# Kernel tuning notes

Hardware: AMD Instinct MI355X
Metric: run time of the kernel (lower is better)

## Reference

```python
import jax, jax.numpy as jnp
import numpy as np

N_HEADS = 8
B, TS, SEG, D, FACTOR, DFF = 4, 64, 128, 256, 10, 1024


def sparsemax(z):
    # projection onto the simplex along the last axis (Martins & Astudillo 2016)
    d = z.shape[-1]
    z_sorted = -jnp.sort(-z, axis=-1)                      # descending
    k = jnp.arange(1, d + 1, dtype=z.dtype)
    z_cum = jnp.cumsum(z_sorted, axis=-1)
    support = (1.0 + k * z_sorted) > z_cum
    k_z = jnp.sum(support.astype(jnp.int32), axis=-1, keepdims=True)
    tau = (jnp.take_along_axis(z_cum, k_z - 1, axis=-1) - 1.0) / k_z.astype(z.dtype)
    return jnp.maximum(z - tau, 0.0)


def _hopf(q_in, k_in, wq, bq, wk, bk, wv, bv, wo, bo):
    # Faithful Hopfield block. NOTE: original torch code ignores the `values`
    # argument -- values are value_projection(key_projection(keys)).
    b, L, _ = q_in.shape
    S = k_in.shape[1]
    q = (q_in @ wq + bq).reshape(b, L, N_HEADS, -1)
    kproj = k_in @ wk + bk
    v = (kproj @ wv + bv).reshape(b, S, N_HEADS, -1)
    kk = kproj.reshape(b, S, N_HEADS, -1)
    scale = 1.0 / np.sqrt(q.shape[-1]).astype(np.float32)
    A = sparsemax(jnp.einsum('blhe,bshe->bhls', q, kk) * scale)
    out = jnp.einsum('bhls,bshd->blhd', A, v)
    # mix=True: transpose(2,1).contiguous().view(B, L, -1) quirk
    out = jnp.swapaxes(out, 1, 2).reshape(b, L, -1)
    return out @ wo + bo


def _mlp(h, w1, b1, w2, b2):
    return jax.nn.gelu(h @ w1 + b1, approximate=False) @ w2 + b2


def _ln(h, g, b, eps=1e-5):
    m = jnp.mean(h, axis=-1, keepdims=True)
    v = jnp.var(h, axis=-1, keepdims=True)
    return (h - m) / jnp.sqrt(v + eps) * g + b


def setup_inputs() -> dict:
    key = jax.random.key(0)
    ks = jax.random.split(key, 24)
    i = 0
    inp = {}
    inp['x'] = jax.random.normal(ks[i], (B, TS, SEG, D), jnp.float32); i += 1
    for pfx in ('ct', 'cs', 'hp'):
        for nm in ('q', 'k', 'v', 'o'):
            inp[f'{pfx}_w{nm}'] = jax.random.normal(ks[i], (D, D), jnp.float32) * 0.02; i += 1
            inp[f'{pfx}_b{nm}'] = jnp.zeros((D,), jnp.float32)
    inp['cs_key'] = jax.random.normal(ks[i], (1, FACTOR, D), jnp.float32) * 0.02; i += 1
    inp['ln_g'] = jnp.ones((D,), jnp.float32)
    inp['ln_b'] = jnp.zeros((D,), jnp.float32)
    for mp in ('mlp1', 'mlp2'):
        inp[f'{mp}_w1'] = jax.random.normal(ks[i], (D, DFF), jnp.float32) * 0.02; i += 1
        inp[f'{mp}_b1'] = jnp.zeros((DFF,), jnp.float32)
        inp[f'{mp}_w2'] = jax.random.normal(ks[i], (DFF, D), jnp.float32) * 0.02; i += 1
        inp[f'{mp}_b2'] = jnp.zeros((D,), jnp.float32)
    return inp


def reference(x, ct_wq, ct_bq, ct_wk, ct_bk, ct_wv, ct_bv, ct_wo, ct_bo,
              cs_wq, cs_bq, cs_wk, cs_bk, cs_wv, cs_bv, cs_wo, cs_bo, cs_key,
              hp_wq, hp_bq, hp_wk, hp_bk, hp_wv, hp_bv, hp_wo, hp_bo,
              ln_g, ln_b, mlp1_w1, mlp1_b1, mlp1_w2, mlp1_b2,
              mlp2_w1, mlp2_b1, mlp2_w2, mlp2_b2):
    b, ts, seg, d = x.shape
    time_in = x.reshape(b * ts, seg, d)
    time_enc = _hopf(time_in, time_in, ct_wq, ct_bq, ct_wk, ct_bk, ct_wv, ct_bv, ct_wo, ct_bo)
    dim_in = time_in + time_enc
    dim_in = dim_in + _mlp(dim_in, mlp1_w1, mlp1_b1, mlp1_w2, mlp1_b2)
    # (b ts) seg d -> (b seg) ts d
    series_in = dim_in.reshape(b, ts, seg, d).transpose(0, 2, 1, 3).reshape(b * seg, ts, d)
    kmat = jnp.broadcast_to(cs_key, (b * seg, cs_key.shape[1], d))
    series_h = _hopf(series_in, kmat, cs_wq, cs_bq, cs_wk, cs_bk, cs_wv, cs_bv, cs_wo, cs_bo)
    # original passes series_h as `values` but Hopfield.forward ignores it
    pooled_h = _hopf(series_in, series_in, hp_wq, hp_bq, hp_wk, hp_bk, hp_wv, hp_bv, hp_wo, hp_bo)
    dim_enc = _ln(series_h + pooled_h, ln_g, ln_b)
    dim_enc = dim_enc + _mlp(dim_enc, mlp2_w1, mlp2_b1, mlp2_w2, mlp2_b2)
    return dim_enc.reshape(b, seg, ts, d).transpose(0, 2, 1, 3)
```

## Files before the change

### kernel.cpp

```cpp
#include <hip/hip_runtime.h>
#include <math.h>


typedef unsigned short u16;
typedef unsigned int u32;
typedef __attribute__((ext_vector_type(8))) short s8v;
typedef __attribute__((ext_vector_type(4))) float f4v;

#define MFMA16 __builtin_amdgcn_mfma_f32_16x16x32_bf16

#define ASYNC16(lds, g) __builtin_amdgcn_global_load_lds( \
    (const __attribute__((address_space(1))) unsigned int*)(const void*)(g), \
    (__attribute__((address_space(3))) unsigned int*)(void*)(lds), 16, 0, 0)

__device__ __forceinline__ float gelu_exact(float x) {
    return 0.5f * x * (1.0f + erff(x * 0.70710678118654752f));
}
__device__ __forceinline__ u16 bf16_rne(float f) {
    u32 u = __float_as_uint(f);
    return (u16)((u + 0x7FFFu + ((u >> 16) & 1u)) >> 16);
}
__device__ __forceinline__ float bf16_to_f(u16 h) {
    return __uint_as_float((u32)h << 16);
}

struct WB {
    const float* src[14];
    u16* dst[14];
    int K[14], N[14];
};
__global__ __launch_bounds__(256)
void wconv_batch(WB wb)
{
    __shared__ float tile[32][33];
    const int mi = blockIdx.y;
    const int K = wb.K[mi], N = wb.N[mi];
    const int tilesN = N >> 5;
    if ((int)blockIdx.x >= tilesN * (K >> 5)) return;
    const int n0 = (blockIdx.x % tilesN) * 32, k0 = (blockIdx.x / tilesN) * 32;
    const float* W = wb.src[mi];
    u16* Wh = wb.dst[mi];
    const int t = threadIdx.x;
    const int r = t >> 3, c = (t & 7) << 2;
    const float4 f = *(const float4*)&W[(size_t)(k0 + r) * N + n0 + c];
    tile[r][c] = f.x; tile[r][c + 1] = f.y; tile[r][c + 2] = f.z; tile[r][c + 3] = f.w;
    __syncthreads();
    u32 hp[2];
    #pragma unroll
    for (int p = 0; p < 2; ++p) {
        const u16 h0 = bf16_rne(tile[c + p * 2][r]);
        const u16 h1 = bf16_rne(tile[c + p * 2 + 1][r]);
        hp[p] = (u32)h0 | ((u32)h1 << 16);
    }
    uint2 hv; hv.x = hp[0]; hv.y = hp[1];
    *(uint2*)&Wh[(size_t)(n0 + r) * K + k0 + c] = hv;
}

__global__ __launch_bounds__(256)
void conv_hi(const float* __restrict__ x, u16* __restrict__ xh)
{
    const size_t base = ((size_t)blockIdx.x * 256 + threadIdx.x) * 8;
    const float4 a = *(const float4*)(x + base);
    const float4 b = *(const float4*)(x + base + 4);
    const float fs[8] = {a.x, a.y, a.z, a.w, b.x, b.y, b.z, b.w};
    __align__(16) u16 hh[8];
    #pragma unroll
    for (int i = 0; i < 8; ++i) hh[i] = bf16_rne(fs[i]);
    *(uint4*)(xh + base) = *(const uint4*)hh;
}

__global__ __launch_bounds__(256)
void bias_concat(const float* a0, const float* a1, float* o1,
                 const float* b0, const float* b1, const float* b2, float* o2)
{
    const int t = threadIdx.x;
    o1[t] = a0[t]; o1[256 + t] = a1[t];
    o2[t] = b0[t]; o2[256 + t] = b1[t]; o2[512 + t] = b2[t];
}

template<int GELU, int RES, int OUTMODE>
__global__ __launch_bounds__(256)
void gemm_bf16(const u16* __restrict__ A, int lda, const u16* __restrict__ W,
               const float* __restrict__ bias, const float* __restrict__ Rf,
               u16* __restrict__ Cb, float* __restrict__ Cf,
               int M, int N, int K)
{
    __shared__ __align__(16) u16 SM[128 * 136];
    u16* const As = SM;
    u16* const Ws = SM + 128 * 64;
    const int t = threadIdx.x;
    const int bm = blockIdx.x, bn = blockIdx.y;
    const int w = t >> 6, lane = t & 63;
    const int wy = w >> 1, wx = w & 1;
    const int lm = lane & 15, quad = lane >> 4, kq = quad << 3;
    const int srow = lane >> 3;
    const int scol = (((lane & 7) ^ srow) << 3);
    const u16* gA = A + (size_t)(bm * 128 + w * 32 + srow) * lda + scol;
    const u16* gW = W + (size_t)(bn * 128 + w * 32 + srow) * K + scol;
    f4v acc[4][4] = {};
    for (int k0 = 0; k0 < K; k0 += 64) {
        #pragma unroll
        for (int r8 = 0; r8 < 4; ++r8) {
            ASYNC16(&As[(w * 32 + r8 * 8) * 64], gA + k0 + (size_t)(r8 * 8) * lda);
            ASYNC16(&Ws[(w * 32 + r8 * 8) * 64], gW + k0 + (size_t)(r8 * 8) * K);
        }
        __syncthreads();
        #pragma unroll
        for (int ks = 0; ks < 2; ++ks) {
            const int ch = ks * 4 + quad;
            const int sw = ((ch ^ (lm & 7)) << 3);
            s8v fw[4], fa[4];
            #pragma unroll
            for (int i = 0; i < 4; ++i) {
                fw[i] = *(const s8v*)&Ws[(wx * 64 + i * 16 + lm) * 64 + sw];
                fa[i] = *(const s8v*)&As[(wy * 64 + i * 16 + lm) * 64 + sw];
            }
            #pragma unroll
            for (int ic = 0; ic < 4; ++ic)
                #pragma unroll
                for (int jr = 0; jr < 4; ++jr)
                    acc[ic][jr] = MFMA16(fw[ic], fa[jr], acc[ic][jr], 0, 0, 0);
        }
        __syncthreads();
    }
    #pragma unroll
    for (int ic = 0; ic < 4; ++ic) {
        const int cloc = wx * 64 + ic * 16 + (quad << 2);
        const int col0 = bn * 128 + cloc;
        const float4 bv = *(const float4*)&bias[col0];
        #pragma unroll
        for (int jr = 0; jr < 4; ++jr) {
            const int rloc = wy * 64 + jr * 16 + lm;
            const int row = bm * 128 + rloc;
            const size_t o = (size_t)row * N + col0;
            float v[4] = {acc[ic][jr][0] + bv.x, acc[ic][jr][1] + bv.y,
                          acc[ic][jr][2] + bv.z, acc[ic][jr][3] + bv.w};
            if (RES) {
                const float4 rv = *(const float4*)(Rf + o);
                v[0] += rv.x; v[1] += rv.y; v[2] += rv.z; v[3] += rv.w;
            }
            if (GELU) {
                #pragma unroll
                for (int r = 0; r < 4; ++r) v[r] = gelu_exact(v[r]);
            }
            if (OUTMODE != 2) {
                uint2 hp;
                hp.x = (u32)bf16_rne(v[0]) | ((u32)bf16_rne(v[1]) << 16);
                hp.y = (u32)bf16_rne(v[2]) | ((u32)bf16_rne(v[3]) << 16);
                *(uint2*)&SM[rloc * 136 + cloc] = hp;
            }
            if (OUTMODE >= 1) {
                float4 fv; fv.x = v[0]; fv.y = v[1]; fv.z = v[2]; fv.w = v[3];
                *(float4*)(Cf + o) = fv;
            }
        }
    }
    if (OUTMODE != 2) {
        __syncthreads();
        #pragma unroll
        for (int p = 0; p < 8; ++p) {
            const int idx = p * 256 + t;
            const int row = idx >> 4, ch = (idx & 15) << 3;
            *(uint4*)&Cb[(size_t)(bm * 128 + row) * N + bn * 128 + ch] =
                *(const uint4*)&SM[row * 136 + ch];
        }
    }
}

__global__ __launch_bounds__(256)
void gemm_tiny(const float* __restrict__ A, const float* __restrict__ W,
               const float* __restrict__ bias, float* __restrict__ Cf,
               u16* __restrict__ Ch, int K, int N)
{
    __shared__ float red[8][33];
    const int m = blockIdx.x;
    const int ncol = blockIdx.y * 32 + (threadIdx.x & 31);
    const int ks = threadIdx.x >> 5;
    const int kc = K >> 3;
    float p = 0.f;
    for (int k = ks * kc; k < (ks + 1) * kc; ++k)
        p = fmaf(A[(size_t)m * K + k], W[(size_t)k * N + ncol], p);
    red[ks][threadIdx.x & 31] = p;
    __syncthreads();
    if (ks == 0) {
        float s = bias[ncol];
        #pragma unroll
        for (int i = 0; i < 8; ++i) s += red[i][threadIdx.x & 31];
        Cf[(size_t)m * N + ncol] = s;
        if (Ch) Ch[(size_t)m * N + ncol] = bf16_rne(s);
    }
}

__global__ __launch_bounds__(256)
void cs_vt(const float* __restrict__ v2f, u16* __restrict__ VT2)
{
    const int c = threadIdx.x;
    for (int j = 0; j < 32; ++j)
        VT2[c * 32 + j] = (j < 10) ? bf16_rne(v2f[(size_t)j * 256 + c]) : (u16)0;
}

template<int S>
__global__ __launch_bounds__(256)
void transpose_vt(const u16* __restrict__ V, u16* __restrict__ VT)
{
    __shared__ __align__(16) u16 Vs[S * 40];
    const int t = threadIdx.x;
    const int nb = blockIdx.x >> 3, h = blockIdx.x & 7;
    for (int idx = t; idx < S * 4; idx += 256) {
        const int row = idx >> 2, ch = idx & 3;
        *(uint4*)&Vs[row * 40 + ch * 8] =
            *(const uint4*)&V[((size_t)nb * S + row) * 256 + h * 32 + ch * 8];
    }
    __syncthreads();
    for (int idx = t; idx < 32 * S / 8; idx += 256) {
        const int e = idx / (S / 8), seg = idx % (S / 8);
        const int j0 = seg * 8;
        __align__(16) u16 tmp[8];
        #pragma unroll
        for (int i = 0; i < 8; ++i) tmp[i] = Vs[(j0 + i) * 40 + e];
        *(uint4*)&VT[(((size_t)nb * 8 + h) * 32 + e) * S + j0] = *(const uint4*)tmp;
    }
}

template<int L, int S, int SHARED>
__global__ __launch_bounds__(256)
void attn_bf16(const u16* __restrict__ q, int ldq, int qcol0,
               const u16* __restrict__ k, int ldk, int kcol0,
               const u16* __restrict__ VT, u16* __restrict__ ho)
{
    constexpr int S16 = (S + 15) & ~15;
    constexpr int S32 = (S + 31) & ~31;
    constexpr int NT = S16 / 16;
    constexpr int KC = S32 / 32;
    constexpr int LC = L / 64;
    constexpr int SP = S32 + 8;
    __shared__ __align__(16) u16 Qs[64 * 32];
    __shared__ __align__(16) u16 Ks[S16 * 32];
    __shared__ __align__(16) u16 Vs[32 * SP];
    __shared__ __align__(16) u16 Ps[64 * SP];
    const int t = threadIdx.x;
    const int lc = (LC == 1) ? 0 : (blockIdx.x & (LC - 1));
    const int bh = (LC == 1) ? blockIdx.x : (blockIdx.x >> 1);
    const int b = bh >> 3, h = bh & 7;
    const int qrow0 = lc * 64;
    const int w = t >> 6, lane = t & 63;
    const int lm = lane & 15, quad = lane >> 4, kq = quad << 3;

    {
        const int srow = lane >> 2, scol = (lane & 3) << 3;
        const u16* g = q + (size_t)(b * L + qrow0 + w * 16 + srow) * ldq
                         + qcol0 + h * 32 + scol;
        ASYNC16(&Qs[(w * 16) * 32], g);
    }
    if (SHARED) {
        for (int idx = t; idx < S16 * 4; idx += 256) {
            const int row = idx >> 2, ch = idx & 3;
            uint4 val = make_uint4(0, 0, 0, 0);
            if (row < S) val = *(const uint4*)&k[(size_t)row * ldk + kcol0 + h * 32 + ch * 8];
            *(uint4*)&Ks[row * 32 + ch * 8] = val;
        }
    } else {
        const int srow = lane >> 2, scol = (lane & 3) << 3;
        for (int c = w; c < S / 16; c += 4) {
            const u16* g = k + (size_t)(b * S + c * 16 + srow) * ldk
                             + kcol0 + h * 32 + scol;
            ASYNC16(&Ks[(c * 16) * 32], g);
        }
    }
    for (int idx = t; idx < 32 * S32 / 8; idx += 256) {
        const int e = idx / (S32 / 8), ch = idx % (S32 / 8);
        const size_t src = SHARED ? ((size_t)(h * 32 + e) * S32 + ch * 8)
                                  : ((((size_t)b * 8 + h) * 32 + e) * S32 + ch * 8);
        *(uint4*)&Vs[e * SP + ch * 8] = *(const uint4*)&VT[src];
    }
    __syncthreads();

    const s8v fq = *(const s8v*)&Qs[(w * 16 + lm) * 32 + kq];
    f4v zac[NT];
    #pragma unroll
    for (int nt = 0; nt < NT; ++nt) {
        const s8v fk = *(const s8v*)&Ks[(nt * 16 + lm) * 32 + kq];
        zac[nt] = MFMA16(fk, fq, f4v{0.f, 0.f, 0.f, 0.f}, 0, 0, 0);
    }
    const float scale = 0.17677669529663687f;
    float z[NT][4];
    #pragma unroll
    for (int nt = 0; nt < NT; ++nt)
        #pragma unroll
        for (int r = 0; r < 4; ++r) {
            float zz = zac[nt][r] * scale;
            if ((S & 15) && nt * 16 + quad * 4 + r >= S) zz = -3.0e38f;
            z[nt][r] = zz;
        }

    float tau = -3.0e38f, kprev = -1.f;
    for (int it = 0; it <= S; ++it) {
        float sum = 0.f;
        int cnt = 0;
        #pragma unroll
        for (int nt = 0; nt < NT; ++nt)
            #pragma unroll
            for (int r = 0; r < 4; ++r) {
                const bool a = z[nt][r] > tau;
                cnt += a;
                sum += a ? z[nt][r] : 0.f;
            }
        sum += __shfl_xor(sum, 16); cnt += __shfl_xor(cnt, 16);
        sum += __shfl_xor(sum, 32); cnt += __shfl_xor(cnt, 32);
        const float fc = (float)cnt;
        const bool anych = (fc != kprev);
        kprev = fc;
        tau = (sum - 1.f) / fc;
        if (__ballot(anych) == 0ULL) break;
    }

    u16* const Prow = &Ps[(w * 16 + lm) * SP];
    #pragma unroll
    for (int nt = 0; nt < NT; ++nt) {
        const u16 p0 = bf16_rne(fmaxf(z[nt][0] - tau, 0.f));
        const u16 p1 = bf16_rne(fmaxf(z[nt][1] - tau, 0.f));
        const u16 p2 = bf16_rne(fmaxf(z[nt][2] - tau, 0.f));
        const u16 p3 = bf16_rne(fmaxf(z[nt][3] - tau, 0.f));
        uint2 hp;
        hp.x = (u32)p0 | ((u32)p1 << 16);
        hp.y = (u32)p2 | ((u32)p3 << 16);
        *(uint2*)&Prow[nt * 16 + quad * 4] = hp;
    }
    if (S16 != S32) {
        uint2 zz; zz.x = 0u; zz.y = 0u;
        *(uint2*)&Prow[S16 + quad * 4] = zz;
    }
    f4v oac[2] = {};
    u16* const Pw = &Ps[(w * 16) * SP];
    #pragma unroll
    for (int kc = 0; kc < KC; ++kc) {
        const s8v fp = *(const s8v*)&Pw[lm * SP + kc * 32 + kq];
        #pragma unroll
        for (int et = 0; et < 2; ++et) {
            const s8v fv = *(const s8v*)&Vs[(et * 16 + lm) * SP + kc * 32 + kq];
            oac[et] = MFMA16(fp, fv, oac[et], 0, 0, 0);
        }
    }
    #pragma unroll
    for (int et = 0; et < 2; ++et)
        #pragma unroll
        for (int r = 0; r < 4; ++r) {
            const int l = qrow0 + w * 16 + quad * 4 + r;
            ho[(((size_t)b * 8 + h) * L + l) * 32 + et * 16 + lm] = bf16_rne(oac[et][r]);
        }
}

__global__ __launch_bounds__(256)
void layernorm_dual(float* __restrict__ x, const float* __restrict__ g,
                    const float* __restrict__ bb, u16* __restrict__ oh)
{
    const int w = threadIdx.x >> 6, lane = threadIdx.x & 63;
    const size_t base = ((size_t)blockIdx.x * 4 + w) * 256 + lane * 4;
    const float4 xv = *(const float4*)&x[base];
    float s  = xv.x + xv.y + xv.z + xv.w;
    float sq = xv.x * xv.x + xv.y * xv.y + xv.z * xv.z + xv.w * xv.w;
    #pragma unroll
    for (int off = 32; off >= 1; off >>= 1) {
        s  += __shfl_xor(s, off);
        sq += __shfl_xor(sq, off);
    }
    const float mean = s * (1.f / 256.f);
    const float var  = sq * (1.f / 256.f) - mean * mean;
    const float rstd = rsqrtf(var + 1e-5f);
    const float4 gv = *(const float4*)&g[lane * 4];
    const float4 bv = *(const float4*)&bb[lane * 4];
    float4 o;
    o.x = (xv.x - mean) * rstd * gv.x + bv.x;
    o.y = (xv.y - mean) * rstd * gv.y + bv.y;
    o.z = (xv.z - mean) * rstd * gv.z + bv.z;
    o.w = (xv.w - mean) * rstd * gv.w + bv.w;
    *(float4*)&x[base] = o;
    uint2 hp;
    hp.x = (u32)bf16_rne(o.x) | ((u32)bf16_rne(o.y) << 16);
    hp.y = (u32)bf16_rne(o.z) | ((u32)bf16_rne(o.w) << 16);
    *(uint2*)(oh + base) = hp;
}

__global__ __launch_bounds__(256)
void transpose_pl(const uint4* __restrict__ in, uint4* __restrict__ out, int d1, int d2)
{
    const size_t idx = (size_t)blockIdx.x * 256 + threadIdx.x;
    const int c = (int)(idx & 31);
    const size_t r = idx >> 5;
    const int j = (int)(r % d2);
    const size_t r2 = r / d2;
    const int i = (int)(r2 % d1);
    const int bb = (int)(r2 / d1);
    out[(((size_t)bb * d2 + j) * d1 + i) * 32 + c] = in[idx];
}

__global__ __launch_bounds__(256)
void transpose_bd(const float4* __restrict__ in, float4* __restrict__ out, int d1, int d2)
{
    const size_t idx = (size_t)blockIdx.x * 256 + threadIdx.x;
    const int c = (int)(idx & 63);
    const size_t r = idx >> 6;
    const int j = (int)(r % d2);
    const size_t r2 = r / d2;
    const int i = (int)(r2 % d1);
    const int bb = (int)(r2 / d1);
    out[(((size_t)bb * d2 + j) * d1 + i) * 64 + c] = in[idx];
}

extern "C" void kernel_launch(void* const* d_in, const int* in_sizes, int n_in,
                              void* d_out, int out_size, void* d_ws, size_t ws_size,
                              hipStream_t stream)
{
    const float* x      = (const float*)d_in[0];
    const float* ct_wq  = (const float*)d_in[1];  const float* ct_bq = (const float*)d_in[2];
    const float* ct_wk  = (const float*)d_in[3];  const float* ct_bk = (const float*)d_in[4];
    const float* ct_wv  = (const float*)d_in[5];  const float* ct_bv = (const float*)d_in[6];
    const float* ct_wo  = (const float*)d_in[7];  const float* ct_bo = (const float*)d_in[8];
    const float* cs_wq  = (const float*)d_in[9];  const float* cs_bq = (const float*)d_in[10];
    const float* cs_wk  = (const float*)d_in[11]; const float* cs_bk = (const float*)d_in[12];
    const float* cs_wv  = (const float*)d_in[13]; const float* cs_bv = (const float*)d_in[14];
    const float* cs_wo  = (const float*)d_in[15]; const float* cs_bo = (const float*)d_in[16];
    const float* hp_wq  = (const float*)d_in[17]; const float* hp_bq = (const float*)d_in[18];
    const float* hp_wk  = (const float*)d_in[19]; const float* hp_bk = (const float*)d_in[20];
    const float* hp_wv  = (const float*)d_in[21]; const float* hp_bv = (const float*)d_in[22];
    const float* hp_wo  = (const float*)d_in[23]; const float* hp_bo = (const float*)d_in[24];
    const float* cs_key = (const float*)d_in[25];
    const float* ln_g   = (const float*)d_in[26]; const float* ln_b   = (const float*)d_in[27];
    const float* m1_w1  = (const float*)d_in[28]; const float* m1_b1  = (const float*)d_in[29];
    const float* m1_w2  = (const float*)d_in[30]; const float* m1_b2  = (const float*)d_in[31];
    const float* m2_w1  = (const float*)d_in[32]; const float* m2_b1  = (const float*)d_in[33];
    const float* m2_w2  = (const float*)d_in[34]; const float* m2_b2  = (const float*)d_in[35];

    const size_t PS = 8388608ULL;
    u16* WS = (u16*)d_ws;
    auto SLOT = [&](int i) { return WS + (size_t)i * PS; };
    u16* WT = WS + 8 * PS;
    u16* Wqk1 = WT;
    u16* Wv1  = Wqk1 + 512 * 256;
    u16* Wo1  = Wv1  + 65536;
    u16* Wqkq = Wo1  + 65536;
    u16* Wv3  = Wqkq + 768 * 256;
    u16* Wo3  = Wv3  + 65536;
    u16* Wo2  = Wo3  + 65536;
    u16* Wm11 = Wo2  + 65536;
    u16* Wm12 = Wm11 + 262144;
    u16* Wm21 = Wm12 + 262144;
    u16* Wm22 = Wm21 + 262144;
    float* bqk1 = (float*)(Wm22 + 262144);
    float* bqkq = bqk1 + 512;
    float* kp2f = bqkq + 768;
    float* v2f  = kp2f + 2560;
    u16* k2h  = (u16*)(v2f + 2560);
    u16* VT2  = k2h + 2560;

    const dim3 blk(256);
    const int M = 32768;

    {
        WB wb;
        const float* s14[14] = {ct_wq, ct_wk, ct_wv, ct_wo, hp_wq, hp_wk, cs_wq,
                                hp_wv, hp_wo, cs_wo, m1_w1, m1_w2, m2_w1, m2_w2};
        u16* d14[14] = {Wqk1, Wqk1 + 65536, Wv1, Wo1, Wqkq, Wqkq + 65536, Wqkq + 131072,
                        Wv3, Wo3, Wo2, Wm11, Wm12, Wm21, Wm22};
        for (int i = 0; i < 14; ++i) {
            wb.src[i] = s14[i]; wb.dst[i] = d14[i];
            wb.K[i] = (i == 11 || i == 13) ? 1024 : 256;
            wb.N[i] = (i == 10 || i == 12) ? 1024 : 256;
        }
        wconv_batch<<<dim3(256, 14), blk, 0, stream>>>(wb);
        bias_concat<<<dim3(1), blk, 0, stream>>>(ct_bq, ct_bk, bqk1, hp_bq, hp_bk, cs_bq, bqkq);
    }

    u16* xh = SLOT(0);
    u16* QK1 = SLOT(1);
    u16* V1 = SLOT(3);
    u16* VT1 = SLOT(4);
    u16* HO1 = SLOT(0);
    float* DIMINf = (float*)SLOT(5);
    u16* DIMINh = SLOT(4);
    u16* H1 = SLOT(0);
    u16* D2h = SLOT(4);
    u16* SER = SLOT(5);
    u16* QKQ = SLOT(0);
    u16* V3 = SLOT(3);
    u16* VT3 = SLOT(4);
    u16* HO3 = SLOT(3);
    float* POOL = (float*)d_out;
    u16* HO2 = SLOT(3);
    float* SUMf = (float*)SLOT(4);
    u16* DEh = SLOT(7);
    u16* H2 = SLOT(0);
    float* FIN = (float*)SLOT(6);

    conv_hi<<<dim3(4096), blk, 0, stream>>>(x, xh);
    gemm_bf16<0,0,0><<<dim3(256, 4), blk, 0, stream>>>(xh, 256, Wqk1, bqk1, nullptr,
                                                       QK1, nullptr, M, 512, 256);
    gemm_bf16<0,0,0><<<dim3(256, 2), blk, 0, stream>>>(QK1 + 256, 512, Wv1, ct_bv, nullptr,
                                                       V1, nullptr, M, 256, 256);
    transpose_vt<128><<<dim3(2048), blk, 0, stream>>>(V1, VT1);
    attn_bf16<128,128,0><<<dim3(4096), blk, 0, stream>>>(QK1, 512, 0, QK1, 512, 256, VT1, HO1);
    gemm_bf16<0,1,1><<<dim3(256, 2), blk, 0, stream>>>(HO1, 256, Wo1, ct_bo, x,
                                                       DIMINh, DIMINf, M, 256, 256);
    gemm_bf16<1,0,0><<<dim3(256, 8), blk, 0, stream>>>(DIMINh, 256, Wm11, m1_b1, nullptr,
                                                       H1, nullptr, M, 1024, 256);
    gemm_bf16<0,1,0><<<dim3(256, 2), blk, 0, stream>>>(H1, 1024, Wm12, m1_b2, DIMINf,
                                                       D2h, nullptr, M, 256, 1024);
    transpose_pl<<<dim3(4096), blk, 0, stream>>>((const uint4*)D2h, (uint4*)SER, 64, 128);
    gemm_bf16<0,0,0><<<dim3(256, 6), blk, 0, stream>>>(SER, 256, Wqkq, bqkq, nullptr,
                                                       QKQ, nullptr, M, 768, 256);
    gemm_bf16<0,0,0><<<dim3(256, 2), blk, 0, stream>>>(QKQ + 256, 768, Wv3, hp_bv, nullptr,
                                                       V3, nullptr, M, 256, 256);
    transpose_vt<64><<<dim3(4096), blk, 0, stream>>>(V3, VT3);
    attn_bf16<64,64,0><<<dim3(4096), blk, 0, stream>>>(QKQ, 768, 0, QKQ, 768, 256, VT3, HO3);
    gemm_bf16<0,0,2><<<dim3(256, 2), blk, 0, stream>>>(HO3, 256, Wo3, hp_bo, nullptr,
                                                       nullptr, POOL, M, 256, 256);
    gemm_tiny<<<dim3(10, 8), blk, 0, stream>>>(cs_key, cs_wk, cs_bk, kp2f, k2h, 256, 256);
    gemm_tiny<<<dim3(10, 8), blk, 0, stream>>>(kp2f, cs_wv, cs_bv, v2f, nullptr, 256, 256);
    cs_vt<<<dim3(1), blk, 0, stream>>>(v2f, VT2);
    attn_bf16<64,10,1><<<dim3(4096), blk, 0, stream>>>(QKQ, 768, 512, k2h, 256, 0, VT2, HO2);
    gemm_bf16<0,1,2><<<dim3(256, 2), blk, 0, stream>>>(HO2, 256, Wo2, cs_bo, POOL,
                                                       nullptr, SUMf, M, 256, 256);
    layernorm_dual<<<dim3(8192), blk, 0, stream>>>(SUMf, ln_g, ln_b, DEh);
    gemm_bf16<1,0,0><<<dim3(256, 8), blk, 0, stream>>>(DEh, 256, Wm21, m2_b1, nullptr,
                                                       H2, nullptr, M, 1024, 256);
    gemm_bf16<0,1,2><<<dim3(256, 2), blk, 0, stream>>>(H2, 1024, Wm22, m2_b2, SUMf,
                                                       nullptr, FIN, M, 256, 1024);
    transpose_bd<<<dim3(8192), blk, 0, stream>>>((const float4*)FIN, (float4*)d_out, 128, 64);
}
```

Before: 570.0 us.

## Fold layout transposes into GEMM epilogues and merge both output projections

The two standalone transpose kernels go away: the MLP1 second GEMM and the final MLP2 GEMM now write rows to permuted positions directly in their epilogues. The two separate output-projection GEMMs (pooled and series Hopfield) are merged into one K=512 GEMM. It reads HO2 and HO3 as a split A operand against concatenated weights and a summed bias. This removes several full-tensor memory passes and two launches, at the cost of scattered-row writes in the epilogue.

```diff
diff --git a/kernel.cpp b/kernel.cpp
--- a/kernel.cpp
+++ b/kernel.cpp
@@ -27,14 +27,14 @@
 struct WB {
     const float* src[14];
     u16* dst[14];
-    int K[14], N[14];
+    int K[14], N[14], LD[14];
 };
 __global__ __launch_bounds__(256)
 void wconv_batch(WB wb)
 {
     __shared__ float tile[32][33];
     const int mi = blockIdx.y;
-    const int K = wb.K[mi], N = wb.N[mi];
+    const int K = wb.K[mi], N = wb.N[mi], LD = wb.LD[mi];
     const int tilesN = N >> 5;
     if ((int)blockIdx.x >= tilesN * (K >> 5)) return;
     const int n0 = (blockIdx.x % tilesN) * 32, k0 = (blockIdx.x / tilesN) * 32;
@@ -53,7 +53,7 @@
         hp[p] = (u32)h0 | ((u32)h1 << 16);
     }
     uint2 hv; hv.x = hp[0]; hv.y = hp[1];
-    *(uint2*)&Wh[(size_t)(n0 + r) * K + k0 + c] = hv;
+    *(uint2*)&Wh[(size_t)(n0 + r) * LD + k0 + c] = hv;
 }
 
 __global__ __launch_bounds__(256)
@@ -71,19 +71,21 @@
 
 __global__ __launch_bounds__(256)
 void bias_concat(const float* a0, const float* a1, float* o1,
-                 const float* b0, const float* b1, const float* b2, float* o2)
+                 const float* b0, const float* b1, const float* b2, float* o2,
+                 const float* c0, const float* c1, float* o3)
 {
     const int t = threadIdx.x;
     o1[t] = a0[t]; o1[256 + t] = a1[t];
     o2[t] = b0[t]; o2[256 + t] = b1[t]; o2[512 + t] = b2[t];
-}
-
-template<int GELU, int RES, int OUTMODE>
+    o3[t] = c0[t] + c1[t];
+}
+
+template<int GELU, int RES, int OUTMODE, int TRS, int ASPLIT>
 __global__ __launch_bounds__(256)
 void gemm_bf16(const u16* __restrict__ A, int lda, const u16* __restrict__ W,
                const float* __restrict__ bias, const float* __restrict__ Rf,
                u16* __restrict__ Cb, float* __restrict__ Cf,
-               int M, int N, int K)
+               int M, int N, int K, const u16* __restrict__ A2)
 {
     __shared__ __align__(16) u16 SM[128 * 136];
     u16* const As = SM;
@@ -95,13 +97,15 @@
     const int lm = lane & 15, quad = lane >> 4, kq = quad << 3;
     const int srow = lane >> 3;
     const int scol = (((lane & 7) ^ srow) << 3);
-    const u16* gA = A + (size_t)(bm * 128 + w * 32 + srow) * lda + scol;
+    const size_t arow = (size_t)(bm * 128 + w * 32 + srow) * lda + scol;
     const u16* gW = W + (size_t)(bn * 128 + w * 32 + srow) * K + scol;
     f4v acc[4][4] = {};
     for (int k0 = 0; k0 < K; k0 += 64) {
+        const u16* gAk = (ASPLIT && k0 >= 256) ? (A2 + arow + (k0 - 256))
+                                               : (A + arow + k0);
         #pragma unroll
         for (int r8 = 0; r8 < 4; ++r8) {
-            ASYNC16(&As[(w * 32 + r8 * 8) * 64], gA + k0 + (size_t)(r8 * 8) * lda);
+            ASYNC16(&As[(w * 32 + r8 * 8) * 64], gAk + (size_t)(r8 * 8) * lda);
             ASYNC16(&Ws[(w * 32 + r8 * 8) * 64], gW + k0 + (size_t)(r8 * 8) * K);
         }
         __syncthreads();
@@ -150,8 +154,11 @@
                 *(uint2*)&SM[rloc * 136 + cloc] = hp;
             }
             if (OUTMODE >= 1) {
+                int prow = row;
+                if (TRS == 1) prow = ((row >> 13) << 13) + ((row & 127) << 6) + ((row >> 7) & 63);
+                if (TRS == 2) prow = ((row >> 13) << 13) + ((row & 63) << 7) + ((row >> 6) & 127);
                 float4 fv; fv.x = v[0]; fv.y = v[1]; fv.z = v[2]; fv.w = v[3];
-                *(float4*)(Cf + o) = fv;
+                *(float4*)(Cf + (size_t)prow * N + col0) = fv;
             }
         }
     }
@@ -160,9 +167,13 @@
         #pragma unroll
         for (int p = 0; p < 8; ++p) {
             const int idx = p * 256 + t;
-            const int row = idx >> 4, ch = (idx & 15) << 3;
-            *(uint4*)&Cb[(size_t)(bm * 128 + row) * N + bn * 128 + ch] =
-                *(const uint4*)&SM[row * 136 + ch];
+            const int rloc = idx >> 4, ch = (idx & 15) << 3;
+            const int row = bm * 128 + rloc;
+            int prow = row;
+            if (TRS == 1) prow = ((row >> 13) << 13) + ((row & 127) << 6) + ((row >> 7) & 63);
+            if (TRS == 2) prow = ((row >> 13) << 13) + ((row & 63) << 7) + ((row >> 6) & 127);
+            *(uint4*)&Cb[(size_t)prow * N + bn * 128 + ch] =
+                *(const uint4*)&SM[rloc * 136 + ch];
         }
     }
 }
@@ -379,32 +390,6 @@
     hp.x = (u32)bf16_rne(o.x) | ((u32)bf16_rne(o.y) << 16);
     hp.y = (u32)bf16_rne(o.z) | ((u32)bf16_rne(o.w) << 16);
     *(uint2*)(oh + base) = hp;
-}
-
-__global__ __launch_bounds__(256)
-void transpose_pl(const uint4* __restrict__ in, uint4* __restrict__ out, int d1, int d2)
-{
-    const size_t idx = (size_t)blockIdx.x * 256 + threadIdx.x;
-    const int c = (int)(idx & 31);
-    const size_t r = idx >> 5;
-    const int j = (int)(r % d2);
-    const size_t r2 = r / d2;
-    const int i = (int)(r2 % d1);
-    const int bb = (int)(r2 / d1);
-    out[(((size_t)bb * d2 + j) * d1 + i) * 32 + c] = in[idx];
-}
-
-__global__ __launch_bounds__(256)
-void transpose_bd(const float4* __restrict__ in, float4* __restrict__ out, int d1, int d2)
-{
-    const size_t idx = (size_t)blockIdx.x * 256 + threadIdx.x;
-    const int c = (int)(idx & 63);
-    const size_t r = idx >> 6;
-    const int j = (int)(r % d2);
-    const size_t r2 = r / d2;
-    const int i = (int)(r2 % d1);
-    const int bb = (int)(r2 / d1);
-    out[(((size_t)bb * d2 + j) * d1 + i) * 64 + c] = in[idx];
 }
 
 extern "C" void kernel_launch(void* const* d_in, const int* in_sizes, int n_in,
@@ -440,15 +425,15 @@
     u16* Wo1  = Wv1  + 65536;
     u16* Wqkq = Wo1  + 65536;
     u16* Wv3  = Wqkq + 768 * 256;
-    u16* Wo3  = Wv3  + 65536;
-    u16* Wo2  = Wo3  + 65536;
-    u16* Wm11 = Wo2  + 65536;
+    u16* Wsum = Wv3  + 65536;
+    u16* Wm11 = Wsum + 131072;
     u16* Wm12 = Wm11 + 262144;
     u16* Wm21 = Wm12 + 262144;
     u16* Wm22 = Wm21 + 262144;
     float* bqk1 = (float*)(Wm22 + 262144);
     float* bqkq = bqk1 + 512;
-    float* kp2f = bqkq + 768;
+    float* bsum = bqkq + 768;
+    float* kp2f = bsum + 256;
     float* v2f  = kp2f + 2560;
     u16* k2h  = (u16*)(v2f + 2560);
     u16* VT2  = k2h + 2560;
@@ -459,16 +444,18 @@
     {
         WB wb;
         const float* s14[14] = {ct_wq, ct_wk, ct_wv, ct_wo, hp_wq, hp_wk, cs_wq,
-                                hp_wv, hp_wo, cs_wo, m1_w1, m1_w2, m2_w1, m2_w2};
+                                hp_wv, cs_wo, hp_wo, m1_w1, m1_w2, m2_w1, m2_w2};
         u16* d14[14] = {Wqk1, Wqk1 + 65536, Wv1, Wo1, Wqkq, Wqkq + 65536, Wqkq + 131072,
-                        Wv3, Wo3, Wo2, Wm11, Wm12, Wm21, Wm22};
+                        Wv3, Wsum, Wsum + 256, Wm11, Wm12, Wm21, Wm22};
         for (int i = 0; i < 14; ++i) {
             wb.src[i] = s14[i]; wb.dst[i] = d14[i];
             wb.K[i] = (i == 11 || i == 13) ? 1024 : 256;
             wb.N[i] = (i == 10 || i == 12) ? 1024 : 256;
+            wb.LD[i] = (i == 8 || i == 9) ? 512 : wb.K[i];
         }
         wconv_batch<<<dim3(256, 14), blk, 0, stream>>>(wb);
-        bias_concat<<<dim3(1), blk, 0, stream>>>(ct_bq, ct_bk, bqk1, hp_bq, hp_bk, cs_bq, bqkq);
+        bias_concat<<<dim3(1), blk, 0, stream>>>(ct_bq, ct_bk, bqk1, hp_bq, hp_bk, cs_bq, bqkq,
+                                                 cs_bo, hp_bo, bsum);
     }
 
     u16* xh = SLOT(0);
@@ -479,51 +466,44 @@
     float* DIMINf = (float*)SLOT(5);
     u16* DIMINh = SLOT(4);
     u16* H1 = SLOT(0);
-    u16* D2h = SLOT(4);
-    u16* SER = SLOT(5);
+    u16* SER = SLOT(4);
     u16* QKQ = SLOT(0);
     u16* V3 = SLOT(3);
     u16* VT3 = SLOT(4);
     u16* HO3 = SLOT(3);
-    float* POOL = (float*)d_out;
-    u16* HO2 = SLOT(3);
+    u16* HO2 = SLOT(7);
     float* SUMf = (float*)SLOT(4);
-    u16* DEh = SLOT(7);
+    u16* DEh = SLOT(6);
     u16* H2 = SLOT(0);
-    float* FIN = (float*)SLOT(6);
 
     conv_hi<<<dim3(4096), blk, 0, stream>>>(x, xh);
-    gemm_bf16<0,0,0><<<dim3(256, 4), blk, 0, stream>>>(xh, 256, Wqk1, bqk1, nullptr,
-                                                       QK1, nullptr, M, 512, 256);
-    gemm_bf16<0,0,0><<<dim3(256, 2), blk, 0, stream>>>(QK1 + 256, 512, Wv1, ct_bv, nullptr,
-                                                       V1, nullptr, M, 256, 256);
+    gemm_bf16<0,0,0,0,0><<<dim3(256, 4), blk, 0, stream>>>(xh, 256, Wqk1, bqk1, nullptr,
+                                                       QK1, nullptr, M, 512, 256, nullptr);
+    gemm_bf16<0,0,0,0,0><<<dim3(256, 2), blk, 0, stream>>>(QK1 + 256, 512, Wv1, ct_bv, nullptr,
+                                                       V1, nullptr, M, 256, 256, nullptr);
     transpose_vt<128><<<dim3(2048), blk, 0, stream>>>(V1, VT1);
     attn_bf16<128,128,0><<<dim3(4096), blk, 0, stream>>>(QK1, 512, 0, QK1, 512, 256, VT1, HO1);
-    gemm_bf16<0,1,1><<<dim3(256, 2), blk, 0, stream>>>(HO1, 256, Wo1, ct_bo, x,
-                                                       DIMINh, DIMINf, M, 256, 256);
-    gemm_bf16<1,0,0><<<dim3(256, 8), blk, 0, stream>>>(DIMINh, 256, Wm11, m1_b1, nullptr,
-                                                       H1, nullptr, M, 1024, 256);
-    gemm_bf16<0,1,0><<<dim3(256, 2), blk, 0, stream>>>(H1, 1024, Wm12, m1_b2, DIMINf,
-                                                       D2h, nullptr, M, 256, 1024);
-    transpose_pl<<<dim3(4096), blk, 0, stream>>>((const uint4*)D2h, (uint4*)SER, 64, 128);
-    gemm_bf16<0,0,0><<<dim3(256, 6), blk, 0, stream>>>(SER, 256, Wqkq, bqkq, nullptr,
-                                                       QKQ, nullptr, M, 768, 256);
-    gemm_bf16<0,0,0><<<dim3(256, 2), blk, 0, stream>>>(QKQ + 256, 768, Wv3, hp_bv, nullptr,
-                                                       V3, nullptr, M, 256, 256);
+    gemm_bf16<0,1,1,0,0><<<dim3(256, 2), blk, 0, stream>>>(HO1, 256, Wo1, ct_bo, x,
+                                                       DIMINh, DIMINf, M, 256, 256, nullptr);
+    gemm_bf16<1,0,0,0,0><<<dim3(256, 8), blk, 0, stream>>>(DIMINh, 256, Wm11, m1_b1, nullptr,
+                                                       H1, nullptr, M, 1024, 256, nullptr);
+    gemm_bf16<0,1,0,1,0><<<dim3(256, 2), blk, 0, stream>>>(H1, 1024, Wm12, m1_b2, DIMINf,
+                                                       SER, nullptr, M, 256, 1024, nullptr);
+    gemm_bf16<0,0,0,0,0><<<dim3(256, 6), blk, 0, stream>>>(SER, 256, Wqkq, bqkq, nullptr,
+                                                       QKQ, nullptr, M, 768, 256, nullptr);
+    gemm_bf16<0,0,0,0,0><<<dim3(256, 2), blk, 0, stream>>>(QKQ + 256, 768, Wv3, hp_bv, nullptr,
+                                                       V3, nullptr, M, 256, 256, nullptr);
     transpose_vt<64><<<dim3(4096), blk, 0, stream>>>(V3, VT3);
     attn_bf16<64,64,0><<<dim3(4096), blk, 0, stream>>>(QKQ, 768, 0, QKQ, 768, 256, VT3, HO3);
-    gemm_bf16<0,0,2><<<dim3(256, 2), blk, 0, stream>>>(HO3, 256, Wo3, hp_bo, nullptr,
-                                                       nullptr, POOL, M, 256, 256);
     gemm_tiny<<<dim3(10, 8), blk, 0, stream>>>(cs_key, cs_wk, cs_bk, kp2f, k2h, 256, 256);
     gemm_tiny<<<dim3(10, 8), blk, 0, stream>>>(kp2f, cs_wv, cs_bv, v2f, nullptr, 256, 256);
     cs_vt<<<dim3(1), blk, 0, stream>>>(v2f, VT2);
     attn_bf16<64,10,1><<<dim3(4096), blk, 0, stream>>>(QKQ, 768, 512, k2h, 256, 0, VT2, HO2);
-    gemm_bf16<0,1,2><<<dim3(256, 2), blk, 0, stream>>>(HO2, 256, Wo2, cs_bo, POOL,
-                                                       nullptr, SUMf, M, 256, 256);
+    gemm_bf16<0,0,2,0,1><<<dim3(256, 2), blk, 0, stream>>>(HO2, 256, Wsum, bsum, nullptr,
+                                                       nullptr, SUMf, M, 256, 512, HO3);
     layernorm_dual<<<dim3(8192), blk, 0, stream>>>(SUMf, ln_g, ln_b, DEh);
-    gemm_bf16<1,0,0><<<dim3(256, 8), blk, 0, stream>>>(DEh, 256, Wm21, m2_b1, nullptr,
-                                                       H2, nullptr, M, 1024, 256);
-    gemm_bf16<0,1,2><<<dim3(256, 2), blk, 0, stream>>>(H2, 1024, Wm22, m2_b2, SUMf,
-                                                       nullptr, FIN, M, 256, 1024);
-    transpose_bd<<<dim3(8192), blk, 0, stream>>>((const float4*)FIN, (float4*)d_out, 128, 64);
-}
+    gemm_bf16<1,0,0,0,0><<<dim3(256, 8), blk, 0, stream>>>(DEh, 256, Wm21, m2_b1, nullptr,
+                                                       H2, nullptr, M, 1024, 256, nullptr);
+    gemm_bf16<0,1,2,2,0><<<dim3(256, 2), blk, 0, stream>>>(H2, 1024, Wm22, m2_b2, SUMf,
+                                                       nullptr, (float*)d_out, M, 256, 1024, nullptr);
+}
```

Measured after the change: 542.0 us. -4.9%, faster.
